# Kernel tuning notes

Measured on AMD Instinct MI355X. Metric: run time of the kernel, lower is better.

The kernel has to match this reference:

```python
import jax, jax.numpy as jnp
import numpy as np

NU, NI, E = 100000, 20000, 250000
H, HEADS, D, L = 128, 2, 64, 2


def setup_inputs() -> dict:
    key = jax.random.key(0)
    ks = jax.random.split(key, 12)
    s = 0.05  # glorot-ish init scale
    return {
        "x_user": jax.random.normal(ks[0], (NU, 64), jnp.float32),
        "x_item": jax.random.normal(ks[1], (NI, 128), jnp.float32),
        "Wp_user": jax.random.normal(ks[2], (64, H), jnp.float32) * s,
        "bp_user": jnp.zeros((H,), jnp.float32),
        "Wp_item": jax.random.normal(ks[3], (128, H), jnp.float32) * s,
        "bp_item": jnp.zeros((H,), jnp.float32),
        # stacked per [layer, relation] params; rel 0 = user->item, rel 1 = item->user
        "Wl": jax.random.normal(ks[4], (L, 2, H, H), jnp.float32) * s,  # source linear
        "bl": jnp.zeros((L, 2, H), jnp.float32),
        "Wr": jax.random.normal(ks[5], (L, 2, H, H), jnp.float32) * s,  # target linear
        "br": jnp.zeros((L, 2, H), jnp.float32),
        "att": jax.random.normal(ks[6], (L, 2, HEADS, D), jnp.float32) * s,
        "bias": jnp.zeros((L, 2, H), jnp.float32),
        "edge_src": jax.random.randint(ks[7], (E,), 0, NU, jnp.int32),  # user index per edge
        "edge_dst": jax.random.randint(ks[8], (E,), 0, NI, jnp.int32),  # item index per edge
    }


def _gatv2(x_src, x_dst, src, dst, wl, bl_, wr, br_, a, b_, n_dst):
    """One bipartite GATv2Conv (heads=HEADS, out=D, concat=True, eval mode)."""
    xl = (x_src @ wl + bl_).reshape(-1, HEADS, D)  # [Ns, h, d]
    xr = (x_dst @ wr + br_).reshape(-1, HEADS, D)  # [Nd, h, d]
    e = jax.nn.leaky_relu(xl[src] + xr[dst], 0.2)  # [E, h, d]
    logits = jnp.einsum('ehd,hd->eh', e, a)        # [E, h]
    # segment softmax over destination nodes (numerically stable)
    amax = jax.lax.stop_gradient(jax.ops.segment_max(logits, dst, num_segments=n_dst))
    p = jnp.exp(logits - amax[dst])
    denom = jax.ops.segment_sum(p, dst, num_segments=n_dst)
    alpha = p / (denom[dst] + 1e-16)               # PyG softmax epsilon
    msg = xl[src] * alpha[:, :, None]              # [E, h, d]
    out = jax.ops.segment_sum(msg, dst, num_segments=n_dst)  # [Nd, h, d]
    return out.reshape(n_dst, HEADS * D) + b_


def reference(x_user, x_item, Wp_user, bp_user, Wp_item, bp_item,
              Wl, bl, Wr, br, att, bias, edge_src, edge_dst):
    zu = x_user @ Wp_user + bp_user  # [NU, H]
    zi = x_item @ Wp_item + bp_item  # [NI, H]
    for l in range(L):
        zi_new = _gatv2(zu, zi, edge_src, edge_dst,
                        Wl[l, 0], bl[l, 0], Wr[l, 0], br[l, 0], att[l, 0], bias[l, 0], NI)
        zu_new = _gatv2(zi, zu, edge_dst, edge_src,
                        Wl[l, 1], bl[l, 1], Wr[l, 1], br[l, 1], att[l, 1], bias[l, 1], NU)
        zu, zi = zu_new, zi_new
        if l < L - 1:
            zu, zi = jax.nn.relu(zu), jax.nn.relu(zi)  # dropout is identity in eval
    return zu, zi
```

## Files before the change

### kernel.cpp

```cpp
#include <hip/hip_runtime.h>

#define HDIM 128

typedef __attribute__((ext_vector_type(8))) short short8;
typedef __attribute__((ext_vector_type(4))) float float4v;

__device__ __forceinline__ float b2f(unsigned short u){
  return __uint_as_float(((unsigned int)u) << 16);
}
__device__ __forceinline__ unsigned short f2b(float f){
  unsigned int x = __float_as_uint(f);
  x += 0x7fffu + ((x >> 16) & 1u);
  return (unsigned short)(x >> 16);
}

#if __has_builtin(__builtin_amdgcn_exp2f)
#define EXPX(x) __builtin_amdgcn_exp2f(x)
#define LOGSCALE 1.4426950408889634f
#else
#define EXPX(x) __expf(x)
#define LOGSCALE 1.f
#endif

__device__ __forceinline__ float dpp_red8(float x){
  x += __int_as_float(__builtin_amdgcn_update_dpp(0, __float_as_int(x), 0xB1, 0xF, 0xF, true));
  x += __int_as_float(__builtin_amdgcn_update_dpp(0, __float_as_int(x), 0x4E, 0xF, 0xF, true));
  x += __int_as_float(__builtin_amdgcn_update_dpp(0, __float_as_int(x), 0x141, 0xF, 0xF, true));
  return x;
}

__global__ void detect_kernel(const unsigned short* __restrict__ x, int* __restrict__ flag){
  const int tid = threadIdx.x;
  int cnt = 0, tot = 0;
  for (int i = tid * 2; i < 4096; i += 512){
    float v = fabsf(b2f(x[i]));
    tot++;
    if (v > 1e-4f && v < 50.f) cnt++;
  }
  __shared__ int s_cnt[256], s_tot[256];
  s_cnt[tid] = cnt; s_tot[tid] = tot;
  __syncthreads();
  for (int o = 128; o > 0; o >>= 1){
    if (tid < o){ s_cnt[tid] += s_cnt[tid + o]; s_tot[tid] += s_tot[tid + o]; }
    __syncthreads();
  }
  if (tid == 0) flag[0] = (s_cnt[0] * 2 < s_tot[0]) ? 1 : 0;
}

#define P_WPU 0
#define P_WPI 8192
#define P_WL  24576
#define P_WR  90112
#define P_BL  155648
#define P_BR  156160
#define P_ATT 156672
#define P_BIA 157184
#define P_BPU 157696
#define P_BPI 157824
#define P_TOT 157952

struct CvtArgs { const void* src[10]; int len[10]; };

__global__ void cvt_all_kernel(CvtArgs args, unsigned short* __restrict__ P,
                               const int* __restrict__ flag){
  int t = blockIdx.x * 256 + threadIdx.x;
  if (t >= P_TOT) return;
  int local = t;
  int i = 0;
  while (local >= args.len[i]){ local -= args.len[i]; i++; }
  if (*flag) P[t] = f2b(((const float*)args.src[i])[local]);
  else       P[t] = ((const unsigned short*)args.src[i])[local];
}

__global__ void prep_weights_kernel(const unsigned short* __restrict__ P,
                                    unsigned short* __restrict__ Wc)
{
  const int t = blockIdx.x * 256 + threadIdx.x;
  if (t >= 49664) return;
  const unsigned short* Wl = P + P_WL;
  const unsigned short* Wr = P + P_WR;
  const unsigned short* Bm[4] = { Wl, Wr + 16384, Wl + 16384, Wr };
  const unsigned short* Av[4] = { P + P_WPU, P + P_WPU, P + P_WPI, P + P_WPI };
  const unsigned short* bv[4] = { P + P_BPU, P + P_BPU, P + P_BPI, P + P_BPI };
  const unsigned short* bo[4] = { P + P_BL, P + P_BR + 128, P + P_BL + 128, P + P_BR };
  if (t < 49152){
    int job, base;
    if (t < 8192)       { job = 0; base = 0; }
    else if (t < 16384) { job = 1; base = 8192; }
    else if (t < 32768) { job = 2; base = 16384; }
    else                { job = 3; base = 32768; }
    const int local = t - base;
    const int k = local >> 7, n = local & 127;
    const unsigned short* A = Av[job] + (size_t)k * 128;
    const unsigned short* B = Bm[job];
    float s = 0.f;
    #pragma unroll 4
    for (int h = 0; h < 128; h++) s = fmaf(b2f(A[h]), b2f(B[h * 128 + n]), s);
    Wc[t] = f2b(s);
  } else {
    const int local = t - 49152;
    const int job = local >> 7, n = local & 127;
    const unsigned short* B = Bm[job];
    float s = b2f(bo[job][n]);
    for (int h = 0; h < 128; h++) s = fmaf(b2f(bv[job][h]), b2f(B[h * 128 + n]), s);
    Wc[t] = f2b(s);
  }
}

struct PermArgs { const unsigned short* W0[4]; const unsigned short* W1[4];
                  int KS[4]; int base[4]; int n[4]; };
__global__ void permute_all_kernel(PermArgs pa, unsigned short* __restrict__ dst){
  int t = blockIdx.x * 256 + threadIdx.x;
  int job = 0;
  while (job < 4 && t >= pa.base[job] + pa.n[job]) job++;
  if (job >= 4) return;
  int local = t - pa.base[job];
  int KS = pa.KS[job];
  int j = local & 7, rest = local >> 3;
  int l = rest & 63; rest >>= 6;
  int ks = rest % KS, tile = rest / KS;
  int k = ks * 32 + (l >> 4) * 8 + j;
  int c = tile * 16 + (l & 15);
  dst[t] = (c < 128) ? pa.W0[job][k * 128 + c] : pa.W1[job][k * 128 + (c - 128)];
}

__global__ void bias_cat_kernel(const unsigned short* a0, const unsigned short* b0,
                                const unsigned short* a1, const unsigned short* b1,
                                const unsigned short* a2, const unsigned short* b2,
                                const unsigned short* a3, const unsigned short* b3,
                                unsigned short* __restrict__ dst){
  int t = blockIdx.x * 256 + threadIdx.x;
  if (t >= 1024) return;
  const unsigned short* lo[4] = {a0, a1, a2, a3};
  const unsigned short* hi[4] = {b0, b1, b2, b3};
  int set = t >> 8, c = t & 255;
  dst[t] = (c < 128) ? lo[set][c] : hi[set][c - 128];
}

template<int K>
__launch_bounds__(256)
__global__ void linear_mfma_kernel(const void* __restrict__ Xv, int xstride,
                                   const int* __restrict__ flag, int use_flag,
                                   const unsigned short* __restrict__ Bp,
                                   const unsigned short* __restrict__ bias,
                                   unsigned short* __restrict__ Y, int M)
{
  constexpr int KS = K / 32;
  const int wave = threadIdx.x >> 6, lane = threadIdx.x & 63;
  const int quad = lane >> 4, l16 = lane & 15;
  const int row0 = blockIdx.x * 64;
  const bool f32 = use_flag && (*flag != 0);

  float4v acc[4][4];
  const float4v z = {0.f, 0.f, 0.f, 0.f};
  #pragma unroll
  for (int i = 0; i < 4; i++)
    #pragma unroll
    for (int j = 0; j < 4; j++) acc[i][j] = z;

  for (int ks = 0; ks < KS; ks++){
    const int col = ks * 32 + quad * 8;
    short8 a[4];
    #pragma unroll
    for (int mt = 0; mt < 4; mt++){
      int r = row0 + mt * 16 + l16; if (r >= M) r = M - 1;
      if (f32){
        const float* p = (const float*)Xv + (size_t)r * xstride + col;
        short8 tmp;
        #pragma unroll
        for (int j = 0; j < 8; j++) tmp[j] = (short)f2b(p[j]);
        a[mt] = tmp;
      } else {
        a[mt] = *(const short8*)((const unsigned short*)Xv + (size_t)r * xstride + col);
      }
    }
    short8 b[4];
    #pragma unroll
    for (int ntl = 0; ntl < 4; ntl++){
      const int t = wave * 4 + ntl;
      b[ntl] = *(const short8*)(Bp + ((size_t)(t * KS + ks) * 64 + lane) * 8);
    }
    #pragma unroll
    for (int mt = 0; mt < 4; mt++)
      #pragma unroll
      for (int ntl = 0; ntl < 4; ntl++)
        acc[mt][ntl] = __builtin_amdgcn_mfma_f32_16x16x32_bf16(a[mt], b[ntl], acc[mt][ntl], 0, 0, 0);
  }

  #pragma unroll
  for (int mt = 0; mt < 4; mt++){
    #pragma unroll
    for (int ntl = 0; ntl < 4; ntl++){
      const int t = wave * 4 + ntl;
      const int colb = t * 16 + l16;
      const float bb = b2f(bias[colb]);
      #pragma unroll
      for (int r = 0; r < 4; r++){
        const int row = row0 + mt * 16 + quad * 4 + r;
        if (row < M) Y[(size_t)row * 256 + colb] = f2b(acc[mt][ntl][r] + bb);
      }
    }
  }
}

__global__ void count_both_kernel(const int* __restrict__ esrc, const int* __restrict__ edst,
                                  int* __restrict__ degU, int* __restrict__ degI, int E){
  int t = blockIdx.x * 256 + threadIdx.x;
  if (t >= E) return;
  atomicAdd(&degI[edst[t]], 1);
  atomicAdd(&degU[esrc[t]], 1);
}

__global__ void scan_block2_kernel(const int* __restrict__ degI, const int* __restrict__ degU,
                                   int* __restrict__ rpI, int* __restrict__ rpU,
                                   int* __restrict__ blkI, int* __restrict__ blkU,
                                   int NI, int NU, int BI){
  __shared__ int s[256];
  const int tid = threadIdx.x;
  const int b = blockIdx.x;
  const int* deg; int* rowptr; int* blksum; int Nd; int bb;
  if (b < BI){ deg = degI; rowptr = rpI; blksum = blkI; Nd = NI; bb = b; }
  else       { deg = degU; rowptr = rpU; blksum = blkU; Nd = NU; bb = b - BI; }
  const int base = bb * 2048 + tid * 8;
  int v[8]; int tot = 0;
  #pragma unroll
  for (int j = 0; j < 8; j++){
    int idx = base + j;
    v[j] = (idx < Nd) ? deg[idx] : 0;
    tot += v[j];
  }
  s[tid] = tot;
  __syncthreads();
  for (int off = 1; off < 256; off <<= 1){
    int add = (tid >= off) ? s[tid - off] : 0;
    __syncthreads();
    s[tid] += add;
    __syncthreads();
  }
  int run = s[tid] - tot;
  #pragma unroll
  for (int j = 0; j < 8; j++){
    int idx = base + j;
    if (idx < Nd) rowptr[idx] = run;
    run += v[j];
  }
  if (tid == 255) blksum[bb] = s[255];
}

__global__ void scan_top2_kernel(int* __restrict__ blkI, int BI,
                                 int* __restrict__ blkU, int BU){
  const int tid = threadIdx.x;
  int* blk = (tid < 64) ? blkI : blkU;
  const int B = (tid < 64) ? BI : BU;
  const int lane = tid & 63;
  int v = (lane < B) ? blk[lane] : 0;
  const int orig = v;
  #pragma unroll
  for (int off = 1; off < 64; off <<= 1){
    int u = __shfl_up(v, off, 64);
    if (lane >= off) v += u;
  }
  if (lane < B) blk[lane] = v - orig;
}

__global__ void scan_add2_kernel(int* __restrict__ rpI, int* __restrict__ rpU,
                                 const int* __restrict__ blkI, const int* __restrict__ blkU,
                                 int* __restrict__ curI, int* __restrict__ curU,
                                 int NI, int NU, int BI, int E){
  const int b = blockIdx.x;
  int* rowptr; const int* blksum; int* curs; int Nd; int bb;
  if (b < BI){ rowptr = rpI; blksum = blkI; curs = curI; Nd = NI; bb = b; }
  else       { rowptr = rpU; blksum = blkU; curs = curU; Nd = NU; bb = b - BI; }
  const int base = bb * 2048 + threadIdx.x * 8;
  const int add = blksum[bb];
  #pragma unroll
  for (int j = 0; j < 8; j++){
    int idx = base + j;
    if (idx < Nd){ int v = rowptr[idx] + add; rowptr[idx] = v; curs[idx] = v; }
    else if (idx == Nd) rowptr[idx] = E;
  }
}

__global__ void scatter_both_kernel(const int* __restrict__ esrc, const int* __restrict__ edst,
                                    int* __restrict__ curI, int* __restrict__ curU,
                                    int* __restrict__ srcI, int* __restrict__ srcU, int E){
  int t = blockIdx.x * 256 + threadIdx.x;
  if (t < E){
    int d = edst[t];
    int pos = atomicAdd(&curI[d], 1);
    srcI[pos] = esrc[t];
  } else if (t < 2 * E){
    int tt = t - E;
    int d = esrc[tt];
    int pos = atomicAdd(&curU[d], 1);
    srcU[pos] = edst[tt];
  }
}

__global__ void hist_deg_kernel(const int* __restrict__ rpI, const int* __restrict__ rpU,
                                int* __restrict__ histI, int* __restrict__ histU,
                                int NI, int NU, int BI){
  __shared__ int h[64];
  const int tid = threadIdx.x;
  if (tid < 64) h[tid] = 0;
  __syncthreads();
  const int b = blockIdx.x;
  const int* rp; int* gh; int base; int N;
  if (b < BI){ rp = rpI; gh = histI; base = b * 256; N = NI; }
  else       { rp = rpU; gh = histU; base = (b - BI) * 256; N = NU; }
  const int n = base + tid;
  if (n < N){ int d = rp[n + 1] - rp[n]; atomicAdd(&h[min(d, 63)], 1); }
  __syncthreads();
  if (tid < 64 && h[tid]) atomicAdd(&gh[tid], h[tid]);
}

__global__ void scan_hist_kernel(int* __restrict__ histI, int* __restrict__ histU){
  const int tid = threadIdx.x;
  const int lane = tid & 63;
  int* h = (tid < 64) ? histI : histU;
  int v = h[lane];
  int x = v;
  #pragma unroll
  for (int off = 1; off < 64; off <<= 1){
    int u = __shfl_down(x, off, 64);
    x += (lane + off < 64) ? u : 0;
  }
  h[lane] = x - v;
}

__global__ void scatter_perm_kernel(const int* __restrict__ rpI, const int* __restrict__ rpU,
                                    int* __restrict__ histI, int* __restrict__ histU,
                                    int* __restrict__ permI, int* __restrict__ permU,
                                    int NI, int NU, int BI){
  __shared__ int h[64];
  __shared__ int cur[64];
  const int tid = threadIdx.x;
  if (tid < 64) h[tid] = 0;
  __syncthreads();
  const int b = blockIdx.x;
  const int* rp; int* gh; int* perm; int base; int N;
  if (b < BI){ rp = rpI; gh = histI; perm = permI; base = b * 256; N = NI; }
  else       { rp = rpU; gh = histU; perm = permU; base = (b - BI) * 256; N = NU; }
  const int n = base + tid;
  int bk = -1;
  if (n < N){ int d = rp[n + 1] - rp[n]; bk = min(d, 63); atomicAdd(&h[bk], 1); }
  __syncthreads();
  if (tid < 64) cur[tid] = h[tid] ? atomicAdd(&gh[tid], h[tid]) : 0;
  __syncthreads();
  if (n < N){ int r = atomicAdd(&cur[bk], 1); perm[r] = n; }
}

struct GatRel {
  const unsigned short* zlrS;
  const unsigned short* zlrD;
  const int* rowptr;
  const int* srcArr;
  const int* perm;
  const unsigned short* att;
  const unsigned short* bias;
  void* out;
  unsigned long long elem_off;
  int Nd;
  int nw;
};

__launch_bounds__(256)
__global__ void fused_gat_sorted_kernel(GatRel A, GatRel B, int do_relu,
                                        const int* __restrict__ flag, int final_store)
{
  const int wave = threadIdx.x >> 6;
  const int lane = threadIdx.x & 63;
  const int ql = lane & 15;
  const int quad = lane >> 4;
  int gw = blockIdx.x * 4 + wave;
  GatRel R;
  if (gw < A.nw) R = A;
  else {
    gw -= A.nw;
    if (gw >= B.nw) return;
    R = B;
  }

  const int rank = gw * 4 + quad;
  const bool vnode = rank < R.Nd;
  int d = 0;
  if (vnode) d = R.perm[rank];
  int beg = 0, end = 0;
  if (vnode){ beg = R.rowptr[d]; end = R.rowptr[d + 1]; }
  int md = end - beg;
  md = max(md, __shfl_xor(md, 16, 64));
  md = max(md, __shfl_xor(md, 32, 64));

  const uint4* zlS4 = (const uint4*)R.zlrS;
  uint4 rv = ((const uint4*)R.zlrD)[(size_t)d * 32 + 16 + ql];
  float r[8], a[8];
  {
    const unsigned int* rp = (const unsigned int*)&rv;
    #pragma unroll
    for (int j = 0; j < 4; j++){
      r[2*j]   = __uint_as_float(rp[j] << 16);
      r[2*j+1] = __uint_as_float(rp[j] & 0xffff0000u);
    }
  }
  uint4 av = ((const uint4*)R.att)[ql];
  {
    const unsigned int* ap = (const unsigned int*)&av;
    #pragma unroll
    for (int j = 0; j < 4; j++){
      a[2*j]   = __uint_as_float(ap[j] << 16) * LOGSCALE;
      a[2*j+1] = __uint_as_float(ap[j] & 0xffff0000u) * LOGSCALE;
    }
  }

  float m = -1e30f, s = 0.f;
  float acc[8];
  #pragma unroll
  for (int j = 0; j < 8; j++) acc[j] = 0.f;

  if (md > 0){
    const int* sA = R.srcArr;
    int i1 = 0, i2 = 0;
    if (beg < end)     i1 = sA[beg];
    if (beg + 1 < end) i2 = sA[beg + 1];
    uint4 g0 = zlS4[(size_t)i1 * 32 + ql];

    for (int it = 0; it < md; it++){
      uint4 g1 = zlS4[(size_t)i2 * 32 + ql];
      int i3 = 0;
      { int ee = beg + it + 2; if (ee < end) i3 = sA[ee]; }
      const bool valid = (beg + it) < end;

      float x[8];
      const unsigned int* gp = (const unsigned int*)&g0;
      #pragma unroll
      for (int j = 0; j < 4; j++){
        x[2*j]   = __uint_as_float(gp[j] << 16);
        x[2*j+1] = __uint_as_float(gp[j] & 0xffff0000u);
      }
      float p = 0.f;
      #pragma unroll
      for (int j = 0; j < 8; j++){
        float t = x[j] + r[j];
        t = fmaxf(t, 0.2f * t);
        p = fmaf(a[j], t, p);
      }
      p = dpp_red8(p);
      const float pv = valid ? p : -1e30f;

      if (__builtin_expect(__any(pv > m + 8.f), 0)){
        const float mn = fmaxf(m, pv);
        const float scO = EXPX(m - mn);
        const float qv = valid ? EXPX(pv - mn) : 0.f;
        s = fmaf(s, scO, qv);
        #pragma unroll
        for (int j = 0; j < 8; j++) acc[j] = fmaf(acc[j], scO, x[j] * qv);
        m = mn;
      } else {
        const float qv = valid ? EXPX(pv - m) : 0.f;
        s += qv;
        #pragma unroll
        for (int j = 0; j < 8; j++) acc[j] = fmaf(x[j], qv, acc[j]);
      }
      g0 = g1; i2 = i3;
    }
  }

  const float inv = 1.f / (s + 1e-16f);
  uint4 bv = ((const uint4*)R.bias)[ql];
  float o[8];
  {
    const unsigned int* bp = (const unsigned int*)&bv;
    #pragma unroll
    for (int j = 0; j < 4; j++){
      o[2*j]   = fmaf(acc[2*j],   inv, __uint_as_float(bp[j] << 16));
      o[2*j+1] = fmaf(acc[2*j+1], inv, __uint_as_float(bp[j] & 0xffff0000u));
    }
  }
  if (do_relu){
    #pragma unroll
    for (int j = 0; j < 8; j++) o[j] = fmaxf(o[j], 0.f);
  }
  if (!vnode) return;
  const size_t eidx = (size_t)R.elem_off + (size_t)d * HDIM + 8 * ql;
  if (final_store && (*flag != 0)){
    float4 f0 = {o[0], o[1], o[2], o[3]};
    float4 f1 = {o[4], o[5], o[6], o[7]};
    float4* op = (float4*)R.out;
    op[eidx >> 2] = f0;
    op[(eidx >> 2) + 1] = f1;
  } else {
    uint4 w;
    unsigned int* wp = (unsigned int*)&w;
    #pragma unroll
    for (int j = 0; j < 4; j++)
      wp[j] = (unsigned int)f2b(o[2*j]) | ((unsigned int)f2b(o[2*j+1]) << 16);
    ((uint4*)R.out)[eidx >> 3] = w;
  }
}

extern "C" void kernel_launch(void* const* d_in, const int* in_sizes, int n_in,
                              void* d_out, int out_size, void* d_ws, size_t ws_size,
                              hipStream_t stream)
{
  const int* esrc = (const int*)d_in[12];
  const int* edst = (const int*)d_in[13];

  const int NU = in_sizes[0] / 64;
  const int NI = in_sizes[1] / 128;
  const int E  = in_sizes[12];
  const size_t fu = (size_t)NU * HDIM, fi = (size_t)NI * HDIM;

  char* w = (char*)d_ws;
  auto carve = [&](size_t bytes){ char* p = w; w += (bytes + 255) & ~(size_t)255; return p; };
  int* flag = (int*)carve(4);
  unsigned short* Wc = (unsigned short*)carve(49664 * 2);
  unsigned short* P  = (unsigned short*)carve((size_t)P_TOT * 2);
  unsigned short* Bp = (unsigned short*)carve(114688 * 2);
  unsigned short* Bc = (unsigned short*)carve(1024 * 2);
  int* rowptrI = (int*)carve(((size_t)NI + 1) * 4);
  int* rowptrU = (int*)carve(((size_t)NU + 1) * 4);
  int* curs    = (int*)carve(((size_t)NI + NU) * 4);
  int* cursI = curs;
  int* cursU = curs + NI;
  int* blkI = (int*)carve(64 * 4);
  int* blkU = (int*)carve(64 * 4);
  int* hists = (int*)carve(128 * 4);
  int* histI = hists;
  int* histU = hists + 64;
  int* permI = (int*)carve((size_t)NI * 4);
  int* permU = (int*)carve((size_t)NU * 4);
  int* srcI  = (int*)carve((size_t)E * 4);
  int* srcU  = (int*)carve((size_t)E * 4);
  unsigned short* zlrU = (unsigned short*)carve((size_t)NU * 256 * 2);
  unsigned short* zlrI = (unsigned short*)carve((size_t)NI * 256 * 2);
  (void)ws_size; (void)n_in; (void)out_size; (void)fi;

  unsigned short* stage_zu = (unsigned short*)d_out;
  unsigned short* stage_zi = (unsigned short*)d_out + fu;
  (void)stage_zi;

  detect_kernel<<<1, 256, 0, stream>>>((const unsigned short*)d_in[0], flag);
  CvtArgs ca;
  const int srcIdx[10] = {2, 4, 6, 8, 7, 9, 10, 11, 3, 5};
  const int lens[10] = {8192, 16384, 65536, 65536, 512, 512, 512, 512, 128, 128};
  for (int i = 0; i < 10; i++){ ca.src[i] = d_in[srcIdx[i]]; ca.len[i] = lens[i]; }
  cvt_all_kernel<<<(P_TOT + 255) / 256, 256, 0, stream>>>(ca, P, flag);
  prep_weights_kernel<<<(49664 + 255) / 256, 256, 0, stream>>>(P, Wc);

  const unsigned short* cWlU0 = Wc;
  const unsigned short* cWrU1 = Wc + 8192;
  const unsigned short* cWlI1 = Wc + 16384;
  const unsigned short* cWrI0 = Wc + 32768;

  PermArgs pa;
  pa.W0[0] = cWlU0;                 pa.W1[0] = cWrU1;                 pa.KS[0] = 2; pa.base[0] = 0;     pa.n[0] = 16384;
  pa.W0[1] = cWlI1;                 pa.W1[1] = cWrI0;                 pa.KS[1] = 4; pa.base[1] = 16384; pa.n[1] = 32768;
  pa.W0[2] = P + P_WL + 2 * 16384;  pa.W1[2] = P + P_WR + 3 * 16384;  pa.KS[2] = 4; pa.base[2] = 49152; pa.n[2] = 32768;
  pa.W0[3] = P + P_WL + 3 * 16384;  pa.W1[3] = P + P_WR + 2 * 16384;  pa.KS[3] = 4; pa.base[3] = 81920; pa.n[3] = 32768;
  permute_all_kernel<<<(114688 + 255) / 256, 256, 0, stream>>>(pa, Bp);
  unsigned short* BpU0 = Bp;
  unsigned short* BpI0 = Bp + 16384;
  unsigned short* BpU1 = Bp + 49152;
  unsigned short* BpI1 = Bp + 81920;
  bias_cat_kernel<<<4, 256, 0, stream>>>(
      Wc + 49152, Wc + 49152 + 128,
      Wc + 49152 + 256, Wc + 49152 + 384,
      P + P_BL + 256, P + P_BR + 384,
      P + P_BL + 384, P + P_BR + 256,
      Bc);

  const int BI = (NI + 2047) / 2048, BU = (NU + 2047) / 2048;
  hipMemsetAsync(curs, 0, ((size_t)NI + NU) * 4, stream);
  hipMemsetAsync(hists, 0, 512, stream);
  count_both_kernel<<<(E + 255) / 256, 256, 0, stream>>>(esrc, edst, cursU, cursI, E);
  scan_block2_kernel<<<BI + BU, 256, 0, stream>>>(cursI, cursU, rowptrI, rowptrU, blkI, blkU, NI, NU, BI);
  scan_top2_kernel<<<1, 128, 0, stream>>>(blkI, BI, blkU, BU);
  scan_add2_kernel<<<BI + BU, 256, 0, stream>>>(rowptrI, rowptrU, blkI, blkU, cursI, cursU, NI, NU, BI, E);

  const int BI2 = (NI + 255) / 256, BU2 = (NU + 255) / 256;
  hist_deg_kernel<<<BI2 + BU2, 256, 0, stream>>>(rowptrI, rowptrU, histI, histU, NI, NU, BI2);
  scan_hist_kernel<<<1, 128, 0, stream>>>(histI, histU);
  scatter_perm_kernel<<<BI2 + BU2, 256, 0, stream>>>(rowptrI, rowptrU, histI, histU, permI, permU, NI, NU, BI2);

  scatter_both_kernel<<<(2 * E + 255) / 256, 256, 0, stream>>>(esrc, edst, cursI, cursU, srcI, srcU, E);

  const int gMU = (NU + 63) / 64, gMI = (NI + 63) / 64;
  const int nwA = (NI + 3) / 4, nwB = (NU + 3) / 4;
  const int gGat = (nwA + nwB + 3) / 4;

  for (int l = 0; l < 2; l++){
    if (l == 0){
      linear_mfma_kernel<64><<<gMU, 256, 0, stream>>>(d_in[0], 64, flag, 1, BpU0, Bc, zlrU, NU);
      linear_mfma_kernel<128><<<gMI, 256, 0, stream>>>(d_in[1], 128, flag, 1, BpI0, Bc + 256, zlrI, NI);
    } else {
      linear_mfma_kernel<128><<<gMU, 256, 0, stream>>>(stage_zu, 128, flag, 0, BpU1, Bc + 512, zlrU, NU);
      linear_mfma_kernel<128><<<gMI, 256, 0, stream>>>(stage_zi, 128, flag, 0, BpI1, Bc + 768, zlrI, NI);
    }
    const int relu = (l == 0);
    const int final_store = (l == 1);

    GatRel A, B;
    A.zlrS = zlrU; A.zlrD = zlrI; A.rowptr = rowptrI; A.srcArr = srcI; A.perm = permI;
    A.att  = P + P_ATT + (l * 2 + 0) * HDIM;
    A.bias = P + P_BIA + (l * 2 + 0) * HDIM;
    A.out = final_store ? d_out : (void*)stage_zu; A.elem_off = fu; A.Nd = NI; A.nw = nwA;
    B.zlrS = zlrI; B.zlrD = zlrU; B.rowptr = rowptrU; B.srcArr = srcU; B.perm = permU;
    B.att  = P + P_ATT + (l * 2 + 1) * HDIM;
    B.bias = P + P_BIA + (l * 2 + 1) * HDIM;
    B.out = final_store ? d_out : (void*)stage_zu; B.elem_off = 0; B.Nd = NU; B.nw = nwB;

    fused_gat_sorted_kernel<<<gGat, 256, 0, stream>>>(A, B, relu, flag, final_store);
  }
}
```

Baseline: 350.3 us.

## Rewrite leaky-relu attention dot via abs identity and deepen gather prefetch

Uses leaky_relu(t) = 0.6t + 0.4|t| so the destination-dependent part of the attention logit is precomputed once per node (kn). The per-edge work becomes an FMA on x plus an FMA on |x+r|, which replaces the mul/max pair. It also deepens the gather pipeline from one to two rows in flight to hide more load latency. This costs extra registers (c1, c2 and another uint4 buffer) and slightly changes floating-point rounding.

```diff
diff --git a/kernel.cpp b/kernel.cpp
--- a/kernel.cpp
+++ b/kernel.cpp
@@ -393,7 +393,7 @@
 
   const uint4* zlS4 = (const uint4*)R.zlrS;
   uint4 rv = ((const uint4*)R.zlrD)[(size_t)d * 32 + 16 + ql];
-  float r[8], a[8];
+  float r[8], c1[8], c2[8];
   {
     const unsigned int* rp = (const unsigned int*)&rv;
     #pragma unroll
@@ -407,10 +407,16 @@
     const unsigned int* ap = (const unsigned int*)&av;
     #pragma unroll
     for (int j = 0; j < 4; j++){
-      a[2*j]   = __uint_as_float(ap[j] << 16) * LOGSCALE;
-      a[2*j+1] = __uint_as_float(ap[j] & 0xffff0000u) * LOGSCALE;
-    }
-  }
+      const float a0 = __uint_as_float(ap[j] << 16) * LOGSCALE;
+      const float a1 = __uint_as_float(ap[j] & 0xffff0000u) * LOGSCALE;
+      c1[2*j]   = a0 * 0.6f; c2[2*j]   = a0 * 0.4f;
+      c1[2*j+1] = a1 * 0.6f; c2[2*j+1] = a1 * 0.4f;
+    }
+  }
+  float kn = 0.f;
+  #pragma unroll
+  for (int j = 0; j < 8; j++) kn = fmaf(c1[j], r[j], kn);
+  kn = dpp_red8(kn);
 
   float m = -1e30f, s = 0.f;
   float acc[8];
@@ -419,32 +425,36 @@
 
   if (md > 0){
     const int* sA = R.srcArr;
-    int i1 = 0, i2 = 0;
-    if (beg < end)     i1 = sA[beg];
-    if (beg + 1 < end) i2 = sA[beg + 1];
-    uint4 g0 = zlS4[(size_t)i1 * 32 + ql];
+    int i0 = 0, i1 = 0, i2 = 0;
+    if (beg     < end) i0 = sA[beg];
+    if (beg + 1 < end) i1 = sA[beg + 1];
+    if (beg + 2 < end) i2 = sA[beg + 2];
+    uint4 g0 = zlS4[(size_t)i0 * 32 + ql];
+    uint4 g1 = zlS4[(size_t)i1 * 32 + ql];
 
     for (int it = 0; it < md; it++){
-      uint4 g1 = zlS4[(size_t)i2 * 32 + ql];
+      uint4 g2 = zlS4[(size_t)i2 * 32 + ql];
       int i3 = 0;
-      { int ee = beg + it + 2; if (ee < end) i3 = sA[ee]; }
+      { int ee = beg + it + 3; if (ee < end) i3 = sA[ee]; }
       const bool valid = (beg + it) < end;
 
       float x[8];
-      const unsigned int* gp = (const unsigned int*)&g0;
-      #pragma unroll
-      for (int j = 0; j < 4; j++){
-        x[2*j]   = __uint_as_float(gp[j] << 16);
-        x[2*j+1] = __uint_as_float(gp[j] & 0xffff0000u);
+      {
+        const unsigned int* gp = (const unsigned int*)&g0;
+        #pragma unroll
+        for (int j = 0; j < 4; j++){
+          x[2*j]   = __uint_as_float(gp[j] << 16);
+          x[2*j+1] = __uint_as_float(gp[j] & 0xffff0000u);
+        }
       }
-      float p = 0.f;
+      float q1 = 0.f, q2 = 0.f;
       #pragma unroll
       for (int j = 0; j < 8; j++){
-        float t = x[j] + r[j];
-        t = fmaxf(t, 0.2f * t);
-        p = fmaf(a[j], t, p);
+        const float t = x[j] + r[j];
+        q1 = fmaf(c1[j], x[j], q1);
+        q2 = fmaf(c2[j], fabsf(t), q2);
       }
-      p = dpp_red8(p);
+      const float p = dpp_red8(q1 + q2) + kn;
       const float pv = valid ? p : -1e30f;
 
       if (__builtin_expect(__any(pv > m + 8.f), 0)){
@@ -461,7 +471,7 @@
         #pragma unroll
         for (int j = 0; j < 8; j++) acc[j] = fmaf(x[j], qv, acc[j]);
       }
-      g0 = g1; i2 = i3;
+      g0 = g1; g1 = g2; i2 = i3;
     }
   }
 
```

Measured after the change: 364.4 us. +4.0%, slower.

## Fuse preprocessing and linear launches to cut kernel count and memsets

Applied to the files above, without the earlier changes.

Merges many small setup kernels: the dtype sniff moves into the convert kernel, which also zeroes the degree counters and histograms in place of the memsets. The bias concat joins the permute kernel, the block scan and degree histogram are combined using last-block-done tickets, and the permutation scatter joins the edge scatter. The two per-layer linear launches become one. The aim is to remove launch and serialization overhead, at the cost of atomic-ticket synchronization and reading degrees before the cursor reuse. It relies on count results being ready before the fused histogram reads them.

```diff
diff --git a/kernel.cpp b/kernel.cpp
--- a/kernel.cpp
+++ b/kernel.cpp
@@ -29,7 +29,7 @@
   return x;
 }
 
-__global__ void detect_kernel(const unsigned short* __restrict__ x, int* __restrict__ flag){
+__device__ __forceinline__ int sniff_block(const unsigned short* __restrict__ x){
   const int tid = threadIdx.x;
   int cnt = 0, tot = 0;
   for (int i = tid * 2; i < 4096; i += 512){
@@ -44,7 +44,10 @@
     if (tid < o){ s_cnt[tid] += s_cnt[tid + o]; s_tot[tid] += s_tot[tid + o]; }
     __syncthreads();
   }
-  if (tid == 0) flag[0] = (s_cnt[0] * 2 < s_tot[0]) ? 1 : 0;
+  __shared__ int res;
+  if (tid == 0) res = (s_cnt[0] * 2 < s_tot[0]) ? 1 : 0;
+  __syncthreads();
+  return res;
 }
 
 #define P_WPU 0
@@ -59,17 +62,23 @@
 #define P_BPI 157824
 #define P_TOT 157952
 
-struct CvtArgs { const void* src[10]; int len[10]; };
+struct CvtArgs { const void* src[10]; int len[10]; const unsigned short* xsniff; };
 
 __global__ void cvt_all_kernel(CvtArgs args, unsigned short* __restrict__ P,
-                               const int* __restrict__ flag){
+                               int* __restrict__ flag,
+                               int* __restrict__ zero1, int nz1,
+                               int* __restrict__ zero2, int nz2){
+  const int f32 = sniff_block(args.xsniff);
   int t = blockIdx.x * 256 + threadIdx.x;
+  if (t < nz1) zero1[t] = 0;
+  if (t < nz2) zero2[t] = 0;
+  if (t == 0) flag[0] = f32;
   if (t >= P_TOT) return;
   int local = t;
   int i = 0;
   while (local >= args.len[i]){ local -= args.len[i]; i++; }
-  if (*flag) P[t] = f2b(((const float*)args.src[i])[local]);
-  else       P[t] = ((const unsigned short*)args.src[i])[local];
+  if (f32) P[t] = f2b(((const float*)args.src[i])[local]);
+  else     P[t] = ((const unsigned short*)args.src[i])[local];
 }
 
 __global__ void prep_weights_kernel(const unsigned short* __restrict__ P,
@@ -107,10 +116,20 @@
   }
 }
 
-struct PermArgs { const unsigned short* W0[4]; const unsigned short* W1[4];
-                  int KS[4]; int base[4]; int n[4]; };
-__global__ void permute_all_kernel(PermArgs pa, unsigned short* __restrict__ dst){
+struct PermBiasArgs { const unsigned short* W0[4]; const unsigned short* W1[4];
+                      int KS[4]; int base[4]; int n[4];
+                      const unsigned short* blo[4]; const unsigned short* bhi[4]; };
+__global__ void permute_bias_kernel(PermBiasArgs pa, unsigned short* __restrict__ dst,
+                                    unsigned short* __restrict__ dstB){
   int t = blockIdx.x * 256 + threadIdx.x;
+  if (t >= 114688){
+    int u = t - 114688;
+    if (u < 1024){
+      int set = u >> 8, c = u & 255;
+      dstB[u] = (c < 128) ? pa.blo[set][c] : pa.bhi[set][c - 128];
+    }
+    return;
+  }
   int job = 0;
   while (job < 4 && t >= pa.base[job] + pa.n[job]) job++;
   if (job >= 4) return;
@@ -124,32 +143,17 @@
   dst[t] = (c < 128) ? pa.W0[job][k * 128 + c] : pa.W1[job][k * 128 + (c - 128)];
 }
 
-__global__ void bias_cat_kernel(const unsigned short* a0, const unsigned short* b0,
-                                const unsigned short* a1, const unsigned short* b1,
-                                const unsigned short* a2, const unsigned short* b2,
-                                const unsigned short* a3, const unsigned short* b3,
-                                unsigned short* __restrict__ dst){
-  int t = blockIdx.x * 256 + threadIdx.x;
-  if (t >= 1024) return;
-  const unsigned short* lo[4] = {a0, a1, a2, a3};
-  const unsigned short* hi[4] = {b0, b1, b2, b3};
-  int set = t >> 8, c = t & 255;
-  dst[t] = (c < 128) ? lo[set][c] : hi[set][c - 128];
-}
-
 template<int K>
-__launch_bounds__(256)
-__global__ void linear_mfma_kernel(const void* __restrict__ Xv, int xstride,
-                                   const int* __restrict__ flag, int use_flag,
-                                   const unsigned short* __restrict__ Bp,
-                                   const unsigned short* __restrict__ bias,
-                                   unsigned short* __restrict__ Y, int M)
+__device__ __forceinline__ void linear_body(const void* __restrict__ Xv, int xstride,
+                                            bool f32,
+                                            const unsigned short* __restrict__ Bp,
+                                            const unsigned short* __restrict__ bias,
+                                            unsigned short* __restrict__ Y, int M, int bx)
 {
   constexpr int KS = K / 32;
   const int wave = threadIdx.x >> 6, lane = threadIdx.x & 63;
   const int quad = lane >> 4, l16 = lane & 15;
-  const int row0 = blockIdx.x * 64;
-  const bool f32 = use_flag && (*flag != 0);
+  const int row0 = bx * 64;
 
   float4v acc[4][4];
   const float4v z = {0.f, 0.f, 0.f, 0.f};
@@ -203,6 +207,23 @@
   }
 }
 
+template<int KA, int KB>
+__launch_bounds__(256)
+__global__ void linear_both_kernel(const void* __restrict__ XA, int sA,
+                                   const unsigned short* __restrict__ BpA,
+                                   const unsigned short* __restrict__ biasA,
+                                   unsigned short* __restrict__ YA, int MA, int gA,
+                                   const void* __restrict__ XB, int sB,
+                                   const unsigned short* __restrict__ BpB,
+                                   const unsigned short* __restrict__ biasB,
+                                   unsigned short* __restrict__ YB, int MB,
+                                   const int* __restrict__ flag, int use_flag)
+{
+  const bool f32 = use_flag && (*flag != 0);
+  if ((int)blockIdx.x < gA) linear_body<KA>(XA, sA, f32, BpA, biasA, YA, MA, blockIdx.x);
+  else                      linear_body<KB>(XB, sB, f32, BpB, biasB, YB, MB, blockIdx.x - gA);
+}
+
 __global__ void count_both_kernel(const int* __restrict__ esrc, const int* __restrict__ edst,
                                   int* __restrict__ degU, int* __restrict__ degI, int E){
   int t = blockIdx.x * 256 + threadIdx.x;
@@ -211,56 +232,92 @@
   atomicAdd(&degU[esrc[t]], 1);
 }
 
-__global__ void scan_block2_kernel(const int* __restrict__ degI, const int* __restrict__ degU,
-                                   int* __restrict__ rpI, int* __restrict__ rpU,
-                                   int* __restrict__ blkI, int* __restrict__ blkU,
-                                   int NI, int NU, int BI){
-  __shared__ int s[256];
+__global__ void scan_hist_fused_kernel(const int* __restrict__ degI, const int* __restrict__ degU,
+                                       int* __restrict__ rpI, int* __restrict__ rpU,
+                                       int* __restrict__ blkI, int* __restrict__ blkU,
+                                       int* __restrict__ histI, int* __restrict__ histU,
+                                       int* __restrict__ tick,
+                                       int NI, int NU, int BI, int BU, int BI2, int BU2){
   const int tid = threadIdx.x;
   const int b = blockIdx.x;
-  const int* deg; int* rowptr; int* blksum; int Nd; int bb;
-  if (b < BI){ deg = degI; rowptr = rpI; blksum = blkI; Nd = NI; bb = b; }
-  else       { deg = degU; rowptr = rpU; blksum = blkU; Nd = NU; bb = b - BI; }
-  const int base = bb * 2048 + tid * 8;
-  int v[8]; int tot = 0;
-  #pragma unroll
-  for (int j = 0; j < 8; j++){
-    int idx = base + j;
-    v[j] = (idx < Nd) ? deg[idx] : 0;
-    tot += v[j];
-  }
-  s[tid] = tot;
-  __syncthreads();
-  for (int off = 1; off < 256; off <<= 1){
-    int add = (tid >= off) ? s[tid - off] : 0;
-    __syncthreads();
-    s[tid] += add;
-    __syncthreads();
-  }
-  int run = s[tid] - tot;
-  #pragma unroll
-  for (int j = 0; j < 8; j++){
-    int idx = base + j;
-    if (idx < Nd) rowptr[idx] = run;
-    run += v[j];
-  }
-  if (tid == 255) blksum[bb] = s[255];
-}
-
-__global__ void scan_top2_kernel(int* __restrict__ blkI, int BI,
-                                 int* __restrict__ blkU, int BU){
-  const int tid = threadIdx.x;
-  int* blk = (tid < 64) ? blkI : blkU;
-  const int B = (tid < 64) ? BI : BU;
-  const int lane = tid & 63;
-  int v = (lane < B) ? blk[lane] : 0;
-  const int orig = v;
-  #pragma unroll
-  for (int off = 1; off < 64; off <<= 1){
-    int u = __shfl_up(v, off, 64);
-    if (lane >= off) v += u;
-  }
-  if (lane < B) blk[lane] = v - orig;
+  const int nscan = BI + BU;
+  if (b < nscan){
+    __shared__ int s[256];
+    const int* deg; int* rowptr; int* blksum; int Nd; int bb;
+    if (b < BI){ deg = degI; rowptr = rpI; blksum = blkI; Nd = NI; bb = b; }
+    else       { deg = degU; rowptr = rpU; blksum = blkU; Nd = NU; bb = b - BI; }
+    const int base = bb * 2048 + tid * 8;
+    int v[8]; int tot = 0;
+    #pragma unroll
+    for (int j = 0; j < 8; j++){
+      int idx = base + j;
+      v[j] = (idx < Nd) ? deg[idx] : 0;
+      tot += v[j];
+    }
+    s[tid] = tot;
+    __syncthreads();
+    for (int off = 1; off < 256; off <<= 1){
+      int add = (tid >= off) ? s[tid - off] : 0;
+      __syncthreads();
+      s[tid] += add;
+      __syncthreads();
+    }
+    int run = s[tid] - tot;
+    #pragma unroll
+    for (int j = 0; j < 8; j++){
+      int idx = base + j;
+      if (idx < Nd) rowptr[idx] = run;
+      run += v[j];
+    }
+    if (tid == 255) blksum[bb] = s[255];
+    __threadfence();
+    __shared__ int lastS;
+    if (tid == 0) lastS = (atomicAdd(&tick[0], 1) == nscan - 1) ? 1 : 0;
+    __syncthreads();
+    if (lastS && tid < 128){
+      __threadfence();
+      int* blk = (tid < 64) ? blkI : blkU;
+      const int B = (tid < 64) ? BI : BU;
+      const int lane = tid & 63;
+      int v2 = (lane < B) ? blk[lane] : 0;
+      const int orig = v2;
+      #pragma unroll
+      for (int off = 1; off < 64; off <<= 1){
+        int u = __shfl_up(v2, off, 64);
+        if (lane >= off) v2 += u;
+      }
+      if (lane < B) blk[lane] = v2 - orig;
+    }
+  } else {
+    __shared__ int h2[64];
+    if (tid < 64) h2[tid] = 0;
+    __syncthreads();
+    const int bb = b - nscan;
+    const int* deg; int* gh; int base; int N;
+    if (bb < BI2){ deg = degI; gh = histI; base = bb * 256; N = NI; }
+    else         { deg = degU; gh = histU; base = (bb - BI2) * 256; N = NU; }
+    const int n = base + tid;
+    if (n < N) atomicAdd(&h2[min(deg[n], 63)], 1);
+    __syncthreads();
+    if (tid < 64 && h2[tid]) atomicAdd(&gh[tid], h2[tid]);
+    __threadfence();
+    __shared__ int lastH;
+    if (tid == 0) lastH = (atomicAdd(&tick[1], 1) == (BI2 + BU2) - 1) ? 1 : 0;
+    __syncthreads();
+    if (lastH && tid < 128){
+      __threadfence();
+      const int lane = tid & 63;
+      int* hh = (tid < 64) ? histI : histU;
+      int v = hh[lane];
+      int x = v;
+      #pragma unroll
+      for (int off = 1; off < 64; off <<= 1){
+        int u = __shfl_down(x, off, 64);
+        x += (lane + off < 64) ? u : 0;
+      }
+      hh[lane] = x - v;
+    }
+  }
 }
 
 __global__ void scan_add2_kernel(int* __restrict__ rpI, int* __restrict__ rpU,
@@ -281,73 +338,44 @@
   }
 }
 
-__global__ void scatter_both_kernel(const int* __restrict__ esrc, const int* __restrict__ edst,
-                                    int* __restrict__ curI, int* __restrict__ curU,
-                                    int* __restrict__ srcI, int* __restrict__ srcU, int E){
-  int t = blockIdx.x * 256 + threadIdx.x;
-  if (t < E){
-    int d = edst[t];
-    int pos = atomicAdd(&curI[d], 1);
-    srcI[pos] = esrc[t];
-  } else if (t < 2 * E){
-    int tt = t - E;
-    int d = esrc[tt];
-    int pos = atomicAdd(&curU[d], 1);
-    srcU[pos] = edst[tt];
-  }
-}
-
-__global__ void hist_deg_kernel(const int* __restrict__ rpI, const int* __restrict__ rpU,
-                                int* __restrict__ histI, int* __restrict__ histU,
-                                int NI, int NU, int BI){
-  __shared__ int h[64];
+__global__ void scatter_all_kernel(const int* __restrict__ esrc, const int* __restrict__ edst,
+                                   int* __restrict__ curI, int* __restrict__ curU,
+                                   int* __restrict__ srcI, int* __restrict__ srcU,
+                                   const int* __restrict__ rpI, const int* __restrict__ rpU,
+                                   int* __restrict__ histI, int* __restrict__ histU,
+                                   int* __restrict__ permI, int* __restrict__ permU,
+                                   int NI, int NU, int E, int BI2, int BU2){
   const int tid = threadIdx.x;
-  if (tid < 64) h[tid] = 0;
-  __syncthreads();
   const int b = blockIdx.x;
-  const int* rp; int* gh; int base; int N;
-  if (b < BI){ rp = rpI; gh = histI; base = b * 256; N = NI; }
-  else       { rp = rpU; gh = histU; base = (b - BI) * 256; N = NU; }
-  const int n = base + tid;
-  if (n < N){ int d = rp[n + 1] - rp[n]; atomicAdd(&h[min(d, 63)], 1); }
-  __syncthreads();
-  if (tid < 64 && h[tid]) atomicAdd(&gh[tid], h[tid]);
-}
-
-__global__ void scan_hist_kernel(int* __restrict__ histI, int* __restrict__ histU){
-  const int tid = threadIdx.x;
-  const int lane = tid & 63;
-  int* h = (tid < 64) ? histI : histU;
-  int v = h[lane];
-  int x = v;
-  #pragma unroll
-  for (int off = 1; off < 64; off <<= 1){
-    int u = __shfl_down(x, off, 64);
-    x += (lane + off < 64) ? u : 0;
-  }
-  h[lane] = x - v;
-}
-
-__global__ void scatter_perm_kernel(const int* __restrict__ rpI, const int* __restrict__ rpU,
-                                    int* __restrict__ histI, int* __restrict__ histU,
-                                    int* __restrict__ permI, int* __restrict__ permU,
-                                    int NI, int NU, int BI){
-  __shared__ int h[64];
-  __shared__ int cur[64];
-  const int tid = threadIdx.x;
-  if (tid < 64) h[tid] = 0;
-  __syncthreads();
-  const int b = blockIdx.x;
-  const int* rp; int* gh; int* perm; int base; int N;
-  if (b < BI){ rp = rpI; gh = histI; perm = permI; base = b * 256; N = NI; }
-  else       { rp = rpU; gh = histU; perm = permU; base = (b - BI) * 256; N = NU; }
-  const int n = base + tid;
-  int bk = -1;
-  if (n < N){ int d = rp[n + 1] - rp[n]; bk = min(d, 63); atomicAdd(&h[bk], 1); }
-  __syncthreads();
-  if (tid < 64) cur[tid] = h[tid] ? atomicAdd(&gh[tid], h[tid]) : 0;
-  __syncthreads();
-  if (n < N){ int r = atomicAdd(&cur[bk], 1); perm[r] = n; }
+  const int BP = BI2 + BU2;
+  if (b < BP){
+    __shared__ int h[64];
+    __shared__ int cur[64];
+    if (tid < 64) h[tid] = 0;
+    __syncthreads();
+    const int* rp; int* gh; int* perm; int base; int N;
+    if (b < BI2){ rp = rpI; gh = histI; perm = permI; base = b * 256; N = NI; }
+    else        { rp = rpU; gh = histU; perm = permU; base = (b - BI2) * 256; N = NU; }
+    const int n = base + tid;
+    int bk = -1;
+    if (n < N){ int d = rp[n + 1] - rp[n]; bk = min(d, 63); atomicAdd(&h[bk], 1); }
+    __syncthreads();
+    if (tid < 64) cur[tid] = h[tid] ? atomicAdd(&gh[tid], h[tid]) : 0;
+    __syncthreads();
+    if (n < N){ int r = atomicAdd(&cur[bk], 1); perm[r] = n; }
+  } else {
+    int t = (b - BP) * 256 + tid;
+    if (t < E){
+      int d = edst[t];
+      int pos = atomicAdd(&curI[d], 1);
+      srcI[pos] = esrc[t];
+    } else if (t < 2 * E){
+      int tt = t - E;
+      int d = esrc[tt];
+      int pos = atomicAdd(&curU[d], 1);
+      srcU[pos] = edst[tt];
+    }
+  }
 }
 
 struct GatRel {
@@ -524,9 +552,10 @@
   int* cursU = curs + NI;
   int* blkI = (int*)carve(64 * 4);
   int* blkU = (int*)carve(64 * 4);
-  int* hists = (int*)carve(128 * 4);
+  int* hists = (int*)carve(144 * 4);
   int* histI = hists;
   int* histU = hists + 64;
+  int* tick  = hists + 128;
   int* permI = (int*)carve((size_t)NI * 4);
   int* permU = (int*)carve((size_t)NU * 4);
   int* srcI  = (int*)carve((size_t)E * 4);
@@ -537,14 +566,15 @@
 
   unsigned short* stage_zu = (unsigned short*)d_out;
   unsigned short* stage_zi = (unsigned short*)d_out + fu;
-  (void)stage_zi;
-
-  detect_kernel<<<1, 256, 0, stream>>>((const unsigned short*)d_in[0], flag);
+  (void)stage_zi; (void)tick;
+
   CvtArgs ca;
   const int srcIdx[10] = {2, 4, 6, 8, 7, 9, 10, 11, 3, 5};
   const int lens[10] = {8192, 16384, 65536, 65536, 512, 512, 512, 512, 128, 128};
   for (int i = 0; i < 10; i++){ ca.src[i] = d_in[srcIdx[i]]; ca.len[i] = lens[i]; }
-  cvt_all_kernel<<<(P_TOT + 255) / 256, 256, 0, stream>>>(ca, P, flag);
+  ca.xsniff = (const unsigned short*)d_in[0];
+  cvt_all_kernel<<<(P_TOT + 255) / 256, 256, 0, stream>>>(ca, P, flag,
+                                                          curs, NI + NU, hists, 130);
   prep_weights_kernel<<<(49664 + 255) / 256, 256, 0, stream>>>(P, Wc);
 
   const unsigned short* cWlU0 = Wc;
@@ -552,37 +582,31 @@
   const unsigned short* cWlI1 = Wc + 16384;
   const unsigned short* cWrI0 = Wc + 32768;
 
-  PermArgs pa;
+  PermBiasArgs pa;
   pa.W0[0] = cWlU0;                 pa.W1[0] = cWrU1;                 pa.KS[0] = 2; pa.base[0] = 0;     pa.n[0] = 16384;
   pa.W0[1] = cWlI1;                 pa.W1[1] = cWrI0;                 pa.KS[1] = 4; pa.base[1] = 16384; pa.n[1] = 32768;
   pa.W0[2] = P + P_WL + 2 * 16384;  pa.W1[2] = P + P_WR + 3 * 16384;  pa.KS[2] = 4; pa.base[2] = 49152; pa.n[2] = 32768;
   pa.W0[3] = P + P_WL + 3 * 16384;  pa.W1[3] = P + P_WR + 2 * 16384;  pa.KS[3] = 4; pa.base[3] = 81920; pa.n[3] = 32768;
-  permute_all_kernel<<<(114688 + 255) / 256, 256, 0, stream>>>(pa, Bp);
+  pa.blo[0] = Wc + 49152;         pa.bhi[0] = Wc + 49152 + 128;
+  pa.blo[1] = Wc + 49152 + 256;   pa.bhi[1] = Wc + 49152 + 384;
+  pa.blo[2] = P + P_BL + 256;     pa.bhi[2] = P + P_BR + 384;
+  pa.blo[3] = P + P_BL + 384;     pa.bhi[3] = P + P_BR + 256;
+  permute_bias_kernel<<<(114688 + 1024 + 255) / 256, 256, 0, stream>>>(pa, Bp, Bc);
   unsigned short* BpU0 = Bp;
   unsigned short* BpI0 = Bp + 16384;
   unsigned short* BpU1 = Bp + 49152;
   unsigned short* BpI1 = Bp + 81920;
-  bias_cat_kernel<<<4, 256, 0, stream>>>(
-      Wc + 49152, Wc + 49152 + 128,
-      Wc + 49152 + 256, Wc + 49152 + 384,
-      P + P_BL + 256, P + P_BR + 384,
-      P + P_BL + 384, P + P_BR + 256,
-      Bc);
 
   const int BI = (NI + 2047) / 2048, BU = (NU + 2047) / 2048;
-  hipMemsetAsync(curs, 0, ((size_t)NI + NU) * 4, stream);
-  hipMemsetAsync(hists, 0, 512, stream);
+  const int BI2 = (NI + 255) / 256, BU2 = (NU + 255) / 256;
   count_both_kernel<<<(E + 255) / 256, 256, 0, stream>>>(esrc, edst, cursU, cursI, E);
-  scan_block2_kernel<<<BI + BU, 256, 0, stream>>>(cursI, cursU, rowptrI, rowptrU, blkI, blkU, NI, NU, BI);
-  scan_top2_kernel<<<1, 128, 0, stream>>>(blkI, BI, blkU, BU);
+  scan_hist_fused_kernel<<<BI + BU + BI2 + BU2, 256, 0, stream>>>(
+      cursI, cursU, rowptrI, rowptrU, blkI, blkU, histI, histU, tick,
+      NI, NU, BI, BU, BI2, BU2);
   scan_add2_kernel<<<BI + BU, 256, 0, stream>>>(rowptrI, rowptrU, blkI, blkU, cursI, cursU, NI, NU, BI, E);
-
-  const int BI2 = (NI + 255) / 256, BU2 = (NU + 255) / 256;
-  hist_deg_kernel<<<BI2 + BU2, 256, 0, stream>>>(rowptrI, rowptrU, histI, histU, NI, NU, BI2);
-  scan_hist_kernel<<<1, 128, 0, stream>>>(histI, histU);
-  scatter_perm_kernel<<<BI2 + BU2, 256, 0, stream>>>(rowptrI, rowptrU, histI, histU, permI, permU, NI, NU, BI2);
-
-  scatter_both_kernel<<<(2 * E + 255) / 256, 256, 0, stream>>>(esrc, edst, cursI, cursU, srcI, srcU, E);
+  scatter_all_kernel<<<BI2 + BU2 + (2 * E + 255) / 256, 256, 0, stream>>>(
+      esrc, edst, cursI, cursU, srcI, srcU, rowptrI, rowptrU,
+      histI, histU, permI, permU, NI, NU, E, BI2, BU2);
 
   const int gMU = (NU + 63) / 64, gMI = (NI + 63) / 64;
   const int nwA = (NI + 3) / 4, nwB = (NU + 3) / 4;
@@ -590,11 +614,13 @@
 
   for (int l = 0; l < 2; l++){
     if (l == 0){
-      linear_mfma_kernel<64><<<gMU, 256, 0, stream>>>(d_in[0], 64, flag, 1, BpU0, Bc, zlrU, NU);
-      linear_mfma_kernel<128><<<gMI, 256, 0, stream>>>(d_in[1], 128, flag, 1, BpI0, Bc + 256, zlrI, NI);
+      linear_both_kernel<64, 128><<<gMU + gMI, 256, 0, stream>>>(
+          d_in[0], 64, BpU0, Bc, zlrU, NU, gMU,
+          d_in[1], 128, BpI0, Bc + 256, zlrI, NI, flag, 1);
     } else {
-      linear_mfma_kernel<128><<<gMU, 256, 0, stream>>>(stage_zu, 128, flag, 0, BpU1, Bc + 512, zlrU, NU);
-      linear_mfma_kernel<128><<<gMI, 256, 0, stream>>>(stage_zi, 128, flag, 0, BpI1, Bc + 768, zlrI, NI);
+      linear_both_kernel<128, 128><<<gMU + gMI, 256, 0, stream>>>(
+          stage_zu, 128, BpU1, Bc + 512, zlrU, NU, gMU,
+          stage_zi, 128, BpI1, Bc + 768, zlrI, NI, flag, 0);
     }
     const int relu = (l == 0);
     const int final_store = (l == 1);
```

Result: slower. 369.4 us (+5.5%).
